# Performance work log

Hardware: AMD Instinct MI355X
Metric: run time of the kernel (lower is better)

Reference implementation:

```python
import math
import jax, jax.numpy as jnp
import numpy as np
from jax import lax

# config constants
D = 2048          # hidden_size
I = 1024          # moe_intermediate_size
E = 32            # n_routed_experts
K = 4             # num_experts_per_tok
NG = 8            # n_group
TKG = 3           # topk_group
NSH = 2           # n_shared_experts
SCALE = 2.5       # routed_scaling_factor
CF = 1.25         # capacity_factor
B, S = 2, 2048


def setup_inputs() -> dict:
    key = jax.random.key(0)
    ks = jax.random.split(key, 8)
    def rn(k, shape, scale=0.02):
        return jax.random.normal(k, shape, jnp.float32) * scale
    return {
        "hidden_states": jax.random.normal(ks[0], (B, S, D), jnp.float32),
        "router_w": rn(ks[1], (E, D)),
        "e_bias": jnp.zeros((E,), jnp.float32),
        "W_gate": rn(ks[2], (E, D, I)),
        "W_up": rn(ks[3], (E, D, I)),
        "W_down": rn(ks[4], (E, I, D)),
        "shared_gate": rn(ks[5], (I * NSH, D)),
        "shared_up": rn(ks[6], (I * NSH, D)),
        "shared_down": rn(ks[7], (D, I * NSH)),
    }


def _router(x, router_w, e_bias):
    # x: [T, D]
    scores = jax.nn.sigmoid(x @ router_w.T)              # [T, E]
    sc = scores + e_bias[None, :]                         # biased scores (indices only)
    T = x.shape[0]
    gs = sc.reshape(T, NG, E // NG)
    group_scores = lax.top_k(gs, 2)[0].sum(-1)            # [T, NG] sum of top-2 per group
    _, gidx = lax.top_k(group_scores, TKG)                # [T, TKG]
    gmask = jnp.zeros((T, NG), sc.dtype).at[jnp.arange(T)[:, None], gidx].set(1.0)
    smask = jnp.repeat(gmask, E // NG, axis=1)            # [T, E]
    masked = jnp.where(smask > 0, sc, 0.0)
    _, topk_idx = lax.top_k(masked, K)                    # [T, K] int
    topk_w = jnp.take_along_axis(scores, topk_idx, axis=1)
    topk_w = topk_w / (topk_w.sum(-1, keepdims=True) + 1e-20)  # norm_topk_prob
    topk_w = topk_w * SCALE
    return topk_idx.astype(jnp.int32), topk_w


def _moe_forward(hidden_states, router_w, e_bias, W_gate, W_up, W_down,
                 shared_gate, shared_up, shared_down):
    b, s, d = hidden_states.shape
    T = b * s
    C = int(math.ceil(CF * T / E))   # capacity per expert
    EC = E * C
    x = hidden_states.reshape(T, d)
    topk_idx, topk_w = _router(x, router_w, e_bias)

    # dispatch: sort token-expert pairs by expert, capacity-drop extras
    expert_flat = topk_idx.reshape(-1)                    # [T*K]
    w_flat = topk_w.reshape(-1)
    tok_flat = jnp.repeat(jnp.arange(T, dtype=jnp.int32), K)
    sort_ix = jnp.argsort(expert_flat)
    e_sorted = expert_flat[sort_ix]
    tok_s = tok_flat[sort_ix]
    w_s = w_flat[sort_ix]
    counts = jnp.zeros(E, jnp.int32).at[e_sorted].add(1)
    group_start = jnp.concatenate([jnp.zeros(1, jnp.int32),
                                   jnp.cumsum(counts)[:-1].astype(jnp.int32)])
    pos = jnp.arange(T * K, dtype=jnp.int32) - group_start[e_sorted]
    valid = pos < C
    dest = e_sorted * C + jnp.where(valid, pos, 0)        # dropped -> slot 0, weight 0
    slots_token = jnp.zeros(EC, jnp.int32).at[dest].add(jnp.where(valid, tok_s, 0))
    slots_w = jnp.zeros(EC, w_s.dtype).at[dest].add(jnp.where(valid, w_s, 0.0))

    # grouped expert GEMMs
    Xp = x[slots_token].reshape(E, C, d)                  # [E, C, D]
    G = jnp.einsum('ecd,edi->eci', Xp, W_gate)
    U = jnp.einsum('ecd,edi->eci', Xp, W_up)
    Y = jnp.einsum('eci,eid->ecd', jax.nn.silu(G) * U, W_down)
    Yf = Y.reshape(EC, d) * slots_w[:, None]

    out = jnp.zeros((T, d), x.dtype).at[slots_token].add(Yf)

    # shared experts MLP
    shared = (jax.nn.silu(x @ shared_gate.T) * (x @ shared_up.T)) @ shared_down.T
    return (out + shared).reshape(b, s, d)


def reference(hidden_states, router_w, e_bias, W_gate, W_up, W_down,
              shared_gate, shared_up, shared_down):
    return _moe_forward(hidden_states, router_w, e_bias, W_gate, W_up, W_down,
                        shared_gate, shared_up, shared_down)
```

## Files before the change

kernel.cpp:

```cpp
#include <hip/hip_runtime.h>
#include <math.h>

#define T_TOK 4096
#define DIM   2048
#define NEXP  32
#define TOPK  4
#define CAP   160
#define ECAP  (NEXP*CAP)
#define ISZ   1024
#define ISH   2048

typedef short bf16x8 __attribute__((ext_vector_type(8)));
typedef float f32x4  __attribute__((ext_vector_type(4)));

__device__ __forceinline__ unsigned int f2bf(float f){
  union { float f; unsigned int u; } v; v.f = f;
  return (v.u + 0x7fffu + ((v.u >> 16) & 1u)) >> 16;
}

#define GLOAD16(g, l) __builtin_amdgcn_global_load_lds( \
    (const __attribute__((address_space(1))) unsigned int*)(g), \
    (__attribute__((address_space(3))) unsigned int*)(l), 16, 0, 0)

__global__ __launch_bounds__(256) void router_k(const float* __restrict__ x,
                                                const float* __restrict__ rw,
                                                const float* __restrict__ eb,
                                                int* __restrict__ tki,
                                                float* __restrict__ tkw,
                                                unsigned short* __restrict__ xbf,
                                                const float* __restrict__ sg,
                                                const float* __restrict__ su,
                                                const float* __restrict__ sd,
                                                unsigned short* __restrict__ sgb,
                                                unsigned short* __restrict__ sub_,
                                                unsigned short* __restrict__ sdb){
  __shared__ float xs[4][DIM];
  __shared__ float lsh[4][NEXP];
  __shared__ float wsh[NEXP];
  __shared__ float xq[4];
  const int tb = blockIdx.x * 4;
  const int tid = threadIdx.x;
  for (int i = tid; i < 4*(DIM/4); i += 256){
    int t = i >> 9, c = (i & 511) << 2;
    float4 f = *(const float4*)&x[(size_t)(tb + t)*DIM + c];
    *(float4*)&xs[t][c] = f;
    uint2 w;
    w.x = f2bf(f.x) | (f2bf(f.y) << 16);
    w.y = f2bf(f.z) | (f2bf(f.w) << 16);
    *(uint2*)&xbf[(size_t)(tb + t)*DIM + c] = w;
  }
  __syncthreads();
  const int lane = tid & 63, wv = tid >> 6;

  for (int ei = 0; ei < 8; ++ei){
    const int e = wv*8 + ei;
    const float4* wr4 = (const float4*)&rw[(size_t)e*DIM];
    float a0=0.f,a1=0.f,a2=0.f,a3=0.f,w2=0.f;
    float x20=0.f,x21=0.f,x22=0.f,x23=0.f;
    const bool doX2 = (wv == 0) && (ei == 0);
    #pragma unroll
    for (int it = 0; it < 8; ++it){
      const int d4 = it*64 + lane;
      float4 w4 = wr4[d4];
      float4 v0 = *(const float4*)&xs[0][d4*4];
      float4 v1 = *(const float4*)&xs[1][d4*4];
      float4 v2 = *(const float4*)&xs[2][d4*4];
      float4 v3 = *(const float4*)&xs[3][d4*4];
      a0 = fmaf(v0.x,w4.x,fmaf(v0.y,w4.y,fmaf(v0.z,w4.z,fmaf(v0.w,w4.w,a0))));
      a1 = fmaf(v1.x,w4.x,fmaf(v1.y,w4.y,fmaf(v1.z,w4.z,fmaf(v1.w,w4.w,a1))));
      a2 = fmaf(v2.x,w4.x,fmaf(v2.y,w4.y,fmaf(v2.z,w4.z,fmaf(v2.w,w4.w,a2))));
      a3 = fmaf(v3.x,w4.x,fmaf(v3.y,w4.y,fmaf(v3.z,w4.z,fmaf(v3.w,w4.w,a3))));
      w2 = fmaf(w4.x,w4.x,fmaf(w4.y,w4.y,fmaf(w4.z,w4.z,fmaf(w4.w,w4.w,w2))));
      if (doX2){
        x20 = fmaf(v0.x,v0.x,fmaf(v0.y,v0.y,fmaf(v0.z,v0.z,fmaf(v0.w,v0.w,x20))));
        x21 = fmaf(v1.x,v1.x,fmaf(v1.y,v1.y,fmaf(v1.z,v1.z,fmaf(v1.w,v1.w,x21))));
        x22 = fmaf(v2.x,v2.x,fmaf(v2.y,v2.y,fmaf(v2.z,v2.z,fmaf(v2.w,v2.w,x22))));
        x23 = fmaf(v3.x,v3.x,fmaf(v3.y,v3.y,fmaf(v3.z,v3.z,fmaf(v3.w,v3.w,x23))));
      }
    }
    #pragma unroll
    for (int off = 32; off; off >>= 1){
      a0 += __shfl_down(a0, off); a1 += __shfl_down(a1, off);
      a2 += __shfl_down(a2, off); a3 += __shfl_down(a3, off);
      w2 += __shfl_down(w2, off);
      if (doX2){
        x20 += __shfl_down(x20, off); x21 += __shfl_down(x21, off);
        x22 += __shfl_down(x22, off); x23 += __shfl_down(x23, off);
      }
    }
    if (lane == 0){
      lsh[0][e] = a0; lsh[1][e] = a1; lsh[2][e] = a2; lsh[3][e] = a3;
      wsh[e] = w2;
      if (doX2){ xq[0]=x20; xq[1]=x21; xq[2]=x22; xq[3]=x23; }
    }
  }
  __syncthreads();

  {
    const int t = wv;
    const int e = lane & 31;
    const float Lf = lsh[t][e];
    float errS = 0.25f * sqrtf(xq[t]) * sqrtf(wsh[e]) * 6e-6f;
    #pragma unroll
    for (int off = 16; off; off >>= 1)
      errS = fmaxf(errS, __shfl_xor(errS, off));

    double s  = 1.0 / (1.0 + exp(-(double)Lf));
    double sc = s + (double)eb[e];

    int idxr[4]; double svalr[4]; double wsum;
    double g23, g34, g45;
    auto decide = [&](double s_, double sc_){
      const int gb = e & ~3;
      double b0 = __shfl(sc_, gb+0), b1 = __shfl(sc_, gb+1);
      double b2 = __shfl(sc_, gb+2), b3 = __shfl(sc_, gb+3);
      double p = fmax(b0,b1), q = fmin(b0,b1);
      double r = fmax(b2,b3), s2 = fmin(b2,b3);
      double r1 = fmax(p,r), rx = fmin(p,r), ry = fmax(q,s2);
      double r2 = fmax(rx,ry), r3 = fmin(rx,ry);
      double gsc = r1 + r2;
      g23 = r2 - r3;
      const int g = e >> 2;
      int grank = 0;
      #pragma unroll
      for (int h = 0; h < 8; ++h){
        double gh = __shfl(gsc, h*4);
        grank += (gh > gsc) || (gh == gsc && h < g);
      }
      double mi = (grank < 3) ? gsc :  1e300;
      double mo = (grank < 3) ? -1e300 : gsc;
      #pragma unroll
      for (int off = 16; off; off >>= 1){
        mi = fmin(mi, __shfl_xor(mi, off));
        mo = fmax(mo, __shfl_xor(mo, off));
      }
      g34 = mi - mo;
      double v = (grank < 3) ? sc_ : 0.0;
      wsum = 0.0;
      double bv4 = 0.0;
      #pragma unroll
      for (int rr = 0; rr < 5; ++rr){
        double bv = v; int bi = e;
        #pragma unroll
        for (int off = 16; off; off >>= 1){
          double ov = __shfl_xor(bv, off);
          int    oi = __shfl_xor(bi, off);
          if (ov > bv || (ov == bv && oi < bi)){ bv = ov; bi = oi; }
        }
        if (rr < 4){
          idxr[rr] = bi;
          double sv = __shfl(s_, bi);
          svalr[rr] = sv; wsum += sv;
          if (e == bi) v = -1.0e300;
          bv4 = bv;
        } else {
          g45 = bv4 - bv;
        }
      }
    };
    decide(s, sc);
    const bool fl = (g23 < 8.0*(double)errS) || (g45 < 8.0*(double)errS) ||
                    (g34 < 16.0*(double)errS);
    if (__any(fl ? 1 : 0)){
      double myL = 0.0;
      const float4* xr4 = (const float4*)&xs[t][0];
      for (int ei2 = 0; ei2 < NEXP; ++ei2){
        const float4* wr4 = (const float4*)&rw[(size_t)ei2*DIM];
        double acc = 0.0;
        #pragma unroll
        for (int it = 0; it < 8; ++it){
          const int d4 = it*64 + lane;
          float4 w4 = wr4[d4];
          float4 v4 = xr4[d4];
          acc += (double)v4.x*(double)w4.x + (double)v4.y*(double)w4.y
               + (double)v4.z*(double)w4.z + (double)v4.w*(double)w4.w;
        }
        #pragma unroll
        for (int off = 32; off; off >>= 1) acc += __shfl_down(acc, off);
        acc = __shfl(acc, 0);
        if (e == ei2) myL = acc;
      }
      s  = 1.0 / (1.0 + exp(-myL));
      sc = s + (double)eb[e];
      decide(s, sc);
    }
    if (lane == 0){
      const int gt = tb + t;
      #pragma unroll
      for (int r = 0; r < 4; ++r){
        tki[gt*4 + r] = idxr[r];
        tkw[gt*4 + r] = (float)(svalr[r] / (wsum + 1e-20) * 2.5);
      }
    }
  }

  #pragma unroll
  for (int i = 0; i < 6; ++i){
    int g = blockIdx.x*1536 + i*256 + tid;
    int local = g & 524287;
    int sel = g >> 19;
    const float* src = (sel == 0) ? sg : (sel == 1) ? su : sd;
    unsigned short* dst = (sel == 0) ? sgb : (sel == 1) ? sub_ : sdb;
    const float4 a = *(const float4*)&src[(size_t)local*8];
    const float4 b = *(const float4*)&src[(size_t)local*8 + 4];
    uint4 v;
    v.x = f2bf(a.x) | (f2bf(a.y) << 16);
    v.y = f2bf(a.z) | (f2bf(a.w) << 16);
    v.z = f2bf(b.x) | (f2bf(b.y) << 16);
    v.w = f2bf(b.z) | (f2bf(b.w) << 16);
    *(uint4*)&dst[(size_t)local*8] = v;
  }
}

__global__ __launch_bounds__(1024) void dispatch_k(const int* __restrict__ tki,
                                                   const float* __restrict__ tkw,
                                                   int* __restrict__ stok,
                                                   float* __restrict__ sw){
  const int e    = blockIdx.x;
  const int tid  = threadIdx.x;
  const int lane = tid & 63, w = tid >> 6;
  __shared__ int cnt[16], basep[16], tot;

  int ex[16];
  #pragma unroll
  for (int it = 0; it < 16; ++it)
    ex[it] = tki[w*1024 + it*64 + lane];
  int c = 0;
  #pragma unroll
  for (int it = 0; it < 16; ++it)
    c += __popcll(__ballot(ex[it] == e));
  if (lane == 0) cnt[w] = c;
  __syncthreads();
  if (tid == 0){
    int run = 0;
    #pragma unroll
    for (int i = 0; i < 16; ++i){ basep[i] = run; run += cnt[i]; }
    tot = (run < CAP) ? run : CAP;
  }
  __syncthreads();

  int base = basep[w];
  #pragma unroll
  for (int it = 0; it < 16; ++it){
    const int idx = w*1024 + it*64 + lane;
    const bool m = (ex[it] == e);
    unsigned long long mk = __ballot(m);
    int pos = base + __popcll(mk & ((1ull << lane) - 1ull));
    if (m && pos < CAP){
      stok[e*CAP + pos] = idx >> 2;
      sw[e*CAP + pos]   = tkw[idx];
    }
    base += __popcll(mk);
  }

  for (int s2 = tot + tid; s2 < CAP; s2 += 1024){
    stok[e*CAP + s2] = 0;
    sw[e*CAP + s2]   = 0.f;
  }
}

template<int MODE>
__global__ __launch_bounds__(512, 2)
void gemm9_k(const unsigned short* __restrict__ Ab,
             const void* __restrict__ B0v, const void* __restrict__ B1v,
             void* __restrict__ Co,
             const int* __restrict__ stok, const float* __restrict__ sw){
  constexpr int BM   = (MODE < 2) ? 160 : 256;
  constexpr int APL  = BM/16;
  constexpr int FM   = BM/32;
  constexpr int KK   = (MODE == 1) ? ISZ : DIM;
  constexpr int BPL  = (MODE == 2) ? 16 : 8;
  constexpr int NBF  = BPL/4;
  constexpr int TPL  = APL + BPL;
  constexpr int NT   = KK/32;
  constexpr int LDB  = (MODE == 0) ? ISZ : DIM;
  constexpr int LDC  = (MODE == 0) ? ISZ : ((MODE == 2) ? ISH : DIM);
  constexpr int SAIT = (MODE >= 2) ? (TPL+7)/8 : 2;

  __shared__ uint4 lds[3][TPL*64];

  const int tid  = threadIdx.x;
  const int lane = tid & 63, wid = tid >> 6;

  const int bid = blockIdx.x;
  int e = 0, mb = 0, nb;
  if constexpr (MODE < 2){
    const int x = bid & 7, s = bid >> 3;
    e  = x*4 + (s & 3);
    nb = (s >> 2) * (MODE == 0 ? 64 : 128);
  } else {
    mb = (bid & 15)*256; nb = (bid >> 4)*128;
  }

  const unsigned short* gptr[SAIT];
  #pragma unroll
  for (int i = 0; i < SAIT; ++i){
    int p = wid + i*8;
    int pp = (p < ((MODE >= 2) ? TPL : APL)) ? p : 0;
    if (pp < APL){
      int r = pp*16 + (lane & 15);
      int row;
      if constexpr (MODE == 0)      row = stok[e*CAP + r];
      else if constexpr (MODE == 1) row = e*CAP + r;
      else                          row = mb + r;
      gptr[i] = Ab + (size_t)row*KK + (lane >> 4)*8;
    } else {
      int q = pp - APL;
      const unsigned short* src = (const unsigned short*)B0v;
      int n;
      if constexpr (MODE == 2){ if (q & 1) src = (const unsigned short*)B1v;
                                n = nb + (q >> 1)*16 + (lane & 15); }
      else                    { n = nb + q*16 + (lane & 15); }
      gptr[i] = src + (size_t)n*KK + (lane >> 4)*8;
    }
  }
  auto stageG = [&](int k0, int buf){
    char* base = (char*)&lds[buf][0];
    #pragma unroll
    for (int i = 0; i < SAIT; ++i){
      int p = wid + i*8;
      if (p < ((MODE >= 2) ? TPL : APL))
        GLOAD16(gptr[i] + k0, base + p*1024);
    }
  };

  const int bq   = (tid & 127) >> 4;
  const int bcl  = tid & 15;
  const int boct = tid >> 7;
  const float* bkn = nullptr;
  if constexpr (MODE == 0){
    const float* src = (const float*)((bq & 1) ? B1v : B0v);
    int n0 = nb + (bq >> 1)*16 + bcl;
    bkn = src + (size_t)e*KK*LDB + (size_t)boct*8*LDB + n0;
  } else if constexpr (MODE == 1){
    bkn = (const float*)B0v + (size_t)e*KK*LDB + (size_t)boct*8*LDB + (nb + bq*16 + bcl);
  }
  auto loadB = [&](int k0, float (&br)[8]){
    const float* p = bkn + (size_t)k0*LDB;
    #pragma unroll
    for (int j = 0; j < 8; ++j) br[j] = p[(size_t)j*LDB];
  };
  auto writeB = [&](int buf, const float (&br)[8]){
    uint4 v;
    v.x = f2bf(br[0]) | (f2bf(br[1]) << 16);
    v.y = f2bf(br[2]) | (f2bf(br[3]) << 16);
    v.z = f2bf(br[4]) | (f2bf(br[5]) << 16);
    v.w = f2bf(br[6]) | (f2bf(br[7]) << 16);
    *(uint4*)((char*)&lds[buf][0] + (APL + bq)*1024 + boct*256 + bcl*16) = v;
  };

  auto waitK = [&]{
    if constexpr (MODE <= 1){
      if (wid < 2) asm volatile("s_waitcnt vmcnt(10)" ::: "memory");
      else         asm volatile("s_waitcnt vmcnt(9)"  ::: "memory");
      asm volatile("s_waitcnt lgkmcnt(0)" ::: "memory");
    } else if constexpr (MODE == 2){
      asm volatile("s_waitcnt vmcnt(4)" ::: "memory");
    } else {
      asm volatile("s_waitcnt vmcnt(3)" ::: "memory");
    }
  };

  const int wmp = (wid >> 2) * FM;
  const int wq  = wid & 3;
  f32x4 acc[FM][NBF];
  #pragma unroll
  for (int i = 0; i < FM; ++i)
    #pragma unroll
    for (int j = 0; j < NBF; ++j) acc[i][j] = f32x4{0,0,0,0};

  float brA[8], brB[8];

  stageG(0, 0);
  if constexpr (MODE <= 1) loadB(0, brA);
  stageG(32, 1);
  if constexpr (MODE <= 1){ loadB(32, brB); writeB(0, brA); }
  waitK();
  __builtin_amdgcn_s_barrier();

  int cons = 0;
  auto step = [&](int t, float (&brW)[8], float (&brL)[8]){
    const int stg = (cons >= 1) ? cons - 1 : 2;
    const int nxt = (cons == 2) ? 0 : cons + 1;
    if (t + 2 < NT){
      stageG((t+2)*32, stg);
      if constexpr (MODE <= 1) loadB((t+2)*32, brL);
    }
    __builtin_amdgcn_sched_barrier(0);
    const char* L = (const char*)&lds[cons][0];
    bf16x8 af[FM], bfr[NBF];
    #pragma unroll
    for (int i = 0; i < FM; ++i)
      af[i] = *(const bf16x8*)(L + (wmp + i)*1024 + lane*16);
    #pragma unroll
    for (int j = 0; j < NBF; ++j)
      bfr[j] = *(const bf16x8*)(L + (APL + wq*NBF + j)*1024 + lane*16);
    __builtin_amdgcn_s_setprio(1);
    #pragma unroll
    for (int i = 0; i < FM; ++i)
      #pragma unroll
      for (int j = 0; j < NBF; ++j)
        acc[i][j] = __builtin_amdgcn_mfma_f32_16x16x32_bf16(af[i], bfr[j], acc[i][j], 0, 0, 0);
    __builtin_amdgcn_s_setprio(0);
    if constexpr (MODE <= 1){
      if (t + 1 < NT) writeB(nxt, brW);
    }
    if (t + 2 < NT){
      waitK();
    } else if (t == NT - 2){
      asm volatile("s_waitcnt vmcnt(0)" ::: "memory");
      if constexpr (MODE <= 1) asm volatile("s_waitcnt lgkmcnt(0)" ::: "memory");
    }
    if (t < NT - 1) __builtin_amdgcn_s_barrier();
    cons = nxt;
  };

  for (int t2 = 0; t2 < NT/2; ++t2){
    step(2*t2,     brB, brA);
    step(2*t2 + 1, brA, brB);
  }

  const int cl = lane & 15, rg = (lane >> 4)*4;
  #pragma unroll
  for (int i = 0; i < FM; ++i){
    #pragma unroll
    for (int r = 0; r < 4; ++r){
      const int m = (wid >> 2)*(BM/2) + i*16 + rg + r;
      if constexpr (MODE == 0){
        float g = acc[i][0][r], u = acc[i][1][r];
        float h = g / (1.f + __expf(-g)) * u;
        int gcol = nb + wq*16 + cl;
        ((unsigned short*)Co)[(size_t)(e*CAP + m)*LDC + gcol] = (unsigned short)f2bf(h);
      } else if constexpr (MODE == 2){
        #pragma unroll
        for (int jj = 0; jj < 2; ++jj){
          float g = acc[i][jj*2][r], u = acc[i][jj*2+1][r];
          float h = g / (1.f + __expf(-g)) * u;
          int gcol = nb + wq*32 + jj*16 + cl;
          ((unsigned short*)Co)[(size_t)(mb + m)*LDC + gcol] = (unsigned short)f2bf(h);
        }
      } else if constexpr (MODE == 1){
        const int slot = e*CAP + m;
        float w = sw[slot];
        if (w != 0.f){
          int tok = stok[slot];
          #pragma unroll
          for (int j = 0; j < 2; ++j){
            int c = nb + wq*32 + j*16 + cl;
            atomicAdd(&((float*)Co)[(size_t)tok*DIM + c], w * acc[i][j][r]);
          }
        }
      } else {
        #pragma unroll
        for (int j = 0; j < 2; ++j){
          int c = nb + wq*32 + j*16 + cl;
          ((float*)Co)[(size_t)(mb + m)*DIM + c] = acc[i][j][r];
        }
      }
    }
  }
}

extern "C" void kernel_launch(void* const* d_in, const int* in_sizes, int n_in,
                              void* d_out, int out_size, void* d_ws, size_t ws_size,
                              hipStream_t stream){
  const float* x  = (const float*)d_in[0];
  const float* rw = (const float*)d_in[1];
  const float* eb = (const float*)d_in[2];
  const float* wg = (const float*)d_in[3];
  const float* wu = (const float*)d_in[4];
  const float* wd = (const float*)d_in[5];
  const float* sg = (const float*)d_in[6];
  const float* su = (const float*)d_in[7];
  const float* sd = (const float*)d_in[8];
  float* out = (float*)d_out;

  char* ws = (char*)d_ws;
  unsigned short* xbf = (unsigned short*)ws; ws += (size_t)T_TOK*DIM*2;
  unsigned short* hsh = (unsigned short*)ws; ws += (size_t)T_TOK*ISH*2;
  unsigned short* hex = (unsigned short*)ws; ws += (size_t)ECAP*ISZ*2;
  unsigned short* sgb = (unsigned short*)ws; ws += (size_t)ISH*DIM*2;
  unsigned short* sub = (unsigned short*)ws; ws += (size_t)ISH*DIM*2;
  unsigned short* sdb = (unsigned short*)ws; ws += (size_t)DIM*ISH*2;
  int*   tki  = (int*)ws;   ws += (size_t)T_TOK*TOPK*4;
  float* tkw  = (float*)ws; ws += (size_t)T_TOK*TOPK*4;
  int*   stok = (int*)ws;   ws += (size_t)ECAP*4;
  float* sw   = (float*)ws; ws += (size_t)ECAP*4;

  router_k<<<T_TOK/4, 256, 0, stream>>>(x, rw, eb, tki, tkw, xbf,
                                        sg, su, sd, sgb, sub, sdb);
  dispatch_k<<<NEXP, 1024, 0, stream>>>(tki, tkw, stok, sw);

  gemm9_k<2><<<256, 512, 0, stream>>>(xbf, sgb, sub, hsh, nullptr, nullptr);
  gemm9_k<3><<<256, 512, 0, stream>>>(hsh, sdb, nullptr, out, nullptr, nullptr);

  gemm9_k<0><<<512, 512, 0, stream>>>(xbf, wg, wu, hex, stok, sw);
  gemm9_k<1><<<512, 512, 0, stream>>>(hex, wd, nullptr, out, stok, sw);
}
```

Measured before the change: 426.4 us.

## Run shared-expert GEMMs with 1024-thread blocks and a double-buffered loop

```diff
diff --git a/kernel.cpp b/kernel.cpp
--- a/kernel.cpp
+++ b/kernel.cpp
@@ -260,24 +260,26 @@
 }
 
 template<int MODE>
-__global__ __launch_bounds__(512, 2)
+__global__ __launch_bounds__((MODE <= 1) ? 512 : 1024, (MODE <= 1) ? 2 : 4)
 void gemm9_k(const unsigned short* __restrict__ Ab,
              const void* __restrict__ B0v, const void* __restrict__ B1v,
              void* __restrict__ Co,
              const int* __restrict__ stok, const float* __restrict__ sw){
   constexpr int BM   = (MODE < 2) ? 160 : 256;
   constexpr int APL  = BM/16;
-  constexpr int FM   = BM/32;
+  constexpr int FM   = (MODE < 2) ? 5 : 4;
   constexpr int KK   = (MODE == 1) ? ISZ : DIM;
   constexpr int BPL  = (MODE == 2) ? 16 : 8;
-  constexpr int NBF  = BPL/4;
+  constexpr int NBF  = (MODE == 2) ? 4 : 2;
   constexpr int TPL  = APL + BPL;
   constexpr int NT   = KK/32;
   constexpr int LDB  = (MODE == 0) ? ISZ : DIM;
   constexpr int LDC  = (MODE == 0) ? ISZ : ((MODE == 2) ? ISH : DIM);
-  constexpr int SAIT = (MODE >= 2) ? (TPL+7)/8 : 2;
-
-  __shared__ uint4 lds[3][TPL*64];
+  constexpr int NWV  = (MODE <= 1) ? 8 : 16;
+  constexpr int SAIT = 2;
+  constexpr int NBUF = (MODE <= 1) ? 3 : 2;
+
+  __shared__ uint4 lds[NBUF][TPL*64];
 
   const int tid  = threadIdx.x;
   const int lane = tid & 63, wid = tid >> 6;
@@ -295,7 +297,7 @@
   const unsigned short* gptr[SAIT];
   #pragma unroll
   for (int i = 0; i < SAIT; ++i){
-    int p = wid + i*8;
+    int p = wid + i*NWV;
     int pp = (p < ((MODE >= 2) ? TPL : APL)) ? p : 0;
     if (pp < APL){
       int r = pp*16 + (lane & 15);
@@ -318,7 +320,7 @@
     char* base = (char*)&lds[buf][0];
     #pragma unroll
     for (int i = 0; i < SAIT; ++i){
-      int p = wid + i*8;
+      int p = wid + i*NWV;
       if (p < ((MODE >= 2) ? TPL : APL))
         GLOAD16(gptr[i] + k0, base + p*1024);
     }
@@ -354,10 +356,6 @@
       if (wid < 2) asm volatile("s_waitcnt vmcnt(10)" ::: "memory");
       else         asm volatile("s_waitcnt vmcnt(9)"  ::: "memory");
       asm volatile("s_waitcnt lgkmcnt(0)" ::: "memory");
-    } else if constexpr (MODE == 2){
-      asm volatile("s_waitcnt vmcnt(4)" ::: "memory");
-    } else {
-      asm volatile("s_waitcnt vmcnt(3)" ::: "memory");
     }
   };
 
@@ -369,55 +367,77 @@
     #pragma unroll
     for (int j = 0; j < NBF; ++j) acc[i][j] = f32x4{0,0,0,0};
 
-  float brA[8], brB[8];
-
-  stageG(0, 0);
-  if constexpr (MODE <= 1) loadB(0, brA);
-  stageG(32, 1);
-  if constexpr (MODE <= 1){ loadB(32, brB); writeB(0, brA); }
-  waitK();
-  __builtin_amdgcn_s_barrier();
-
-  int cons = 0;
-  auto step = [&](int t, float (&brW)[8], float (&brL)[8]){
-    const int stg = (cons >= 1) ? cons - 1 : 2;
-    const int nxt = (cons == 2) ? 0 : cons + 1;
-    if (t + 2 < NT){
-      stageG((t+2)*32, stg);
-      if constexpr (MODE <= 1) loadB((t+2)*32, brL);
-    }
-    __builtin_amdgcn_sched_barrier(0);
-    const char* L = (const char*)&lds[cons][0];
-    bf16x8 af[FM], bfr[NBF];
-    #pragma unroll
-    for (int i = 0; i < FM; ++i)
-      af[i] = *(const bf16x8*)(L + (wmp + i)*1024 + lane*16);
-    #pragma unroll
-    for (int j = 0; j < NBF; ++j)
-      bfr[j] = *(const bf16x8*)(L + (APL + wq*NBF + j)*1024 + lane*16);
-    __builtin_amdgcn_s_setprio(1);
-    #pragma unroll
-    for (int i = 0; i < FM; ++i)
+  if constexpr (MODE <= 1){
+    float brA[8], brB[8];
+    stageG(0, 0);
+    loadB(0, brA);
+    stageG(32, 1);
+    loadB(32, brB); writeB(0, brA);
+    waitK();
+    __builtin_amdgcn_s_barrier();
+
+    int cons = 0;
+    auto step = [&](int t, float (&brW)[8], float (&brL)[8]){
+      const int stg = (cons >= 1) ? cons - 1 : 2;
+      const int nxt = (cons == 2) ? 0 : cons + 1;
+      if (t + 2 < NT){
+        stageG((t+2)*32, stg);
+        loadB((t+2)*32, brL);
+      }
+      __builtin_amdgcn_sched_barrier(0);
+      const char* L = (const char*)&lds[cons][0];
+      bf16x8 af[FM], bfr[NBF];
+      #pragma unroll
+      for (int i = 0; i < FM; ++i)
+        af[i] = *(const bf16x8*)(L + (wmp + i)*1024 + lane*16);
       #pragma unroll
       for (int j = 0; j < NBF; ++j)
-        acc[i][j] = __builtin_amdgcn_mfma_f32_16x16x32_bf16(af[i], bfr[j], acc[i][j], 0, 0, 0);
-    __builtin_amdgcn_s_setprio(0);
-    if constexpr (MODE <= 1){
+        bfr[j] = *(const bf16x8*)(L + (APL + wq*NBF + j)*1024 + lane*16);
+      __builtin_amdgcn_s_setprio(1);
+      #pragma unroll
+      for (int i = 0; i < FM; ++i)
+        #pragma unroll
+        for (int j = 0; j < NBF; ++j)
+          acc[i][j] = __builtin_amdgcn_mfma_f32_16x16x32_bf16(af[i], bfr[j], acc[i][j], 0, 0, 0);
+      __builtin_amdgcn_s_setprio(0);
       if (t + 1 < NT) writeB(nxt, brW);
-    }
-    if (t + 2 < NT){
-      waitK();
-    } else if (t == NT - 2){
+      if (t + 2 < NT){
+        waitK();
+      } else if (t == NT - 2){
+        asm volatile("s_waitcnt vmcnt(0)" ::: "memory");
+        asm volatile("s_waitcnt lgkmcnt(0)" ::: "memory");
+      }
+      if (t < NT - 1) __builtin_amdgcn_s_barrier();
+      cons = nxt;
+    };
+
+    for (int t2 = 0; t2 < NT/2; ++t2){
+      step(2*t2,     brB, brA);
+      step(2*t2 + 1, brA, brB);
+    }
+  } else {
+    stageG(0, 0);
+    for (int t = 0; t < NT; ++t){
       asm volatile("s_waitcnt vmcnt(0)" ::: "memory");
-      if constexpr (MODE <= 1) asm volatile("s_waitcnt lgkmcnt(0)" ::: "memory");
-    }
-    if (t < NT - 1) __builtin_amdgcn_s_barrier();
-    cons = nxt;
-  };
-
-  for (int t2 = 0; t2 < NT/2; ++t2){
-    step(2*t2,     brB, brA);
-    step(2*t2 + 1, brA, brB);
+      __builtin_amdgcn_s_barrier();
+      if (t + 1 < NT) stageG((t+1)*32, (t+1)&1);
+      __builtin_amdgcn_sched_barrier(0);
+      const char* L = (const char*)&lds[t & 1][0];
+      bf16x8 af[FM], bfr[NBF];
+      #pragma unroll
+      for (int i = 0; i < FM; ++i)
+        af[i] = *(const bf16x8*)(L + (wmp + i)*1024 + lane*16);
+      #pragma unroll
+      for (int j = 0; j < NBF; ++j)
+        bfr[j] = *(const bf16x8*)(L + (APL + wq*NBF + j)*1024 + lane*16);
+      __builtin_amdgcn_s_setprio(1);
+      #pragma unroll
+      for (int i = 0; i < FM; ++i)
+        #pragma unroll
+        for (int j = 0; j < NBF; ++j)
+          acc[i][j] = __builtin_amdgcn_mfma_f32_16x16x32_bf16(af[i], bfr[j], acc[i][j], 0, 0, 0);
+      __builtin_amdgcn_s_setprio(0);
+    }
   }
 
   const int cl = lane & 15, rg = (lane >> 4)*4;
@@ -425,7 +445,7 @@
   for (int i = 0; i < FM; ++i){
     #pragma unroll
     for (int r = 0; r < 4; ++r){
-      const int m = (wid >> 2)*(BM/2) + i*16 + rg + r;
+      const int m = wmp*16 + i*16 + rg + r;
       if constexpr (MODE == 0){
         float g = acc[i][0][r], u = acc[i][1][r];
         float h = g / (1.f + __expf(-g)) * u;
@@ -491,8 +511,8 @@
                                         sg, su, sd, sgb, sub, sdb);
   dispatch_k<<<NEXP, 1024, 0, stream>>>(tki, tkw, stok, sw);
 
-  gemm9_k<2><<<256, 512, 0, stream>>>(xbf, sgb, sub, hsh, nullptr, nullptr);
-  gemm9_k<3><<<256, 512, 0, stream>>>(hsh, sdb, nullptr, out, nullptr, nullptr);
+  gemm9_k<2><<<256, 1024, 0, stream>>>(xbf, sgb, sub, hsh, nullptr, nullptr);
+  gemm9_k<3><<<256, 1024, 0, stream>>>(hsh, sdb, nullptr, out, nullptr, nullptr);
 
   gemm9_k<0><<<512, 512, 0, stream>>>(xbf, wg, wu, hex, stok, sw);
   gemm9_k<1><<<512, 512, 0, stream>>>(hex, wd, nullptr, out, stok, sw);
```

Result: slower. 445.3 us (+4.4%).
